# Kernel optimization log

Hardware: AMD Instinct MI355X
Metric: run time of the kernel (lower is better)

## Reference

```python
import jax, jax.numpy as jnp
import numpy as np
import math

DIM = 2048
NUM_HEADS = 32
HEAD_DIM = DIM // NUM_HEADS  # 64; HEAD_DIM//2 == NUM_HEADS (required by original rope broadcasting)
SEQ_LEN = 2048
BATCH = 2
ROPE_BASE = 10000.0


def apply_rope(inputs, positions):
    # Faithful to original: positions is [L]; sinusoid broadcasts to [1, L, H/2, 1]
    # and then multiplies [B, L, N, H/2] -- the original code relies on N == H/2.
    head_dim = inputs.shape[-1]
    fraction = 2.0 * jnp.arange(head_dim // 2, dtype=inputs.dtype) / head_dim
    timescale = ROPE_BASE ** fraction                      # [H/2]
    sinusoid = positions[:, None] / timescale[None, None, :]  # [1, L, H/2]
    sinusoid = sinusoid[..., None]                         # [1, L, H/2, 1]
    sin = jnp.sin(sinusoid)
    cos = jnp.cos(sinusoid)
    first, second = jnp.split(inputs, 2, axis=-1)          # each [B, L, N, H/2]
    return jnp.concatenate([first * cos - second * sin,
                            second * cos + first * sin], axis=-1)


def setup_inputs() -> dict:
    key = jax.random.key(0)
    ks = jax.random.split(key, 9)
    s = 0.02
    inp = {
        'x': jax.random.normal(ks[0], (BATCH, SEQ_LEN, DIM), dtype=jnp.float32),
        'wq_w': jax.random.normal(ks[1], (DIM, DIM), dtype=jnp.float32) * s,
        'wq_b': jnp.zeros((DIM,), dtype=jnp.float32),
        'wk_w': jax.random.normal(ks[2], (DIM, DIM), dtype=jnp.float32) * s,
        'wk_b': jnp.zeros((DIM,), dtype=jnp.float32),
        'wv_w': jax.random.normal(ks[3], (DIM, DIM), dtype=jnp.float32) * s,
        'wv_b': jnp.zeros((DIM,), dtype=jnp.float32),
        'wo_w': jax.random.normal(ks[4], (DIM, DIM), dtype=jnp.float32) * s,
        'wo_b': jnp.zeros((DIM,), dtype=jnp.float32),
    }
    return inp


def reference(x, wq_w, wq_b, wk_w, wk_b, wv_w, wv_b, wo_w, wo_b):
    B, L, _ = x.shape
    N, H = NUM_HEADS, HEAD_DIM
    q = (x @ wq_w.T + wq_b).reshape(B, L, N, H)
    k = (x @ wk_w.T + wk_b).reshape(B, L, N, H)
    v = (x @ wv_w.T + wv_b).reshape(B, L, N, H)
    positions = jnp.arange(L, dtype=x.dtype)
    q = apply_rope(q, positions)
    k = apply_rope(k, positions)
    # [B, N, L, H]
    q = q.transpose(0, 2, 1, 3)
    k = k.transpose(0, 2, 1, 3)
    v = v.transpose(0, 2, 1, 3)
    scale = math.sqrt(H)
    scores = jnp.einsum('bnqh,bnkh->bnqk', q, k) / scale   # [B, N, L, L]
    causal = jnp.tril(jnp.ones((L, L), dtype=bool))
    scores = jnp.where(causal[None, None], scores, -jnp.inf)
    attn = jax.nn.softmax(scores, axis=-1)
    context = jnp.einsum('bnqk,bnkh->bnqh', attn, v)        # [B, N, L, H]
    context = context.transpose(0, 2, 1, 3).reshape(B, L, DIM)
    return context @ wo_w.T + wo_b
```

## Files before the change

### kernel.cpp

```cpp
#include <hip/hip_runtime.h>
#include <stdint.h>

#define D_MODEL 2048
#define SEQLEN  2048

typedef float f32x4  __attribute__((ext_vector_type(4)));
typedef float f32x16 __attribute__((ext_vector_type(16)));
typedef int   i32x4  __attribute__((ext_vector_type(4)));
typedef short s16x4  __attribute__((ext_vector_type(4)));
typedef __bf16 bf16x8 __attribute__((ext_vector_type(8)));

__device__ __forceinline__ unsigned short f2bf(float f) {
  union { float f; uint32_t u; } x; x.f = f;
  uint32_t r = (x.u + 0x7FFFu + ((x.u >> 16) & 1u)) >> 16;
  return (unsigned short)r;
}

__device__ __forceinline__ uint32_t cvtpk(float lo, float hi) {
  uint32_t r;
  asm("v_cvt_pk_bf16_f32 %0, %1, %2" : "=v"(r) : "v"(lo), "v"(hi));
  return r;
}

__device__ __forceinline__ bf16x8 as_bf16x8(i32x4 v) {
  union { i32x4 i; bf16x8 b; } u; u.i = v; return u.b;
}

#define MFMA16(acc, a, b) \
  acc = __builtin_amdgcn_mfma_f32_16x16x32_bf16(as_bf16x8(a), as_bf16x8(b), acc, 0, 0, 0)
#define MFMA32(acc, a, b) \
  acc = __builtin_amdgcn_mfma_f32_32x32x16_bf16(as_bf16x8(a), as_bf16x8(b), acc, 0, 0, 0)

__device__ __forceinline__ void gload16(const void* g, void* lds) {
  __builtin_amdgcn_global_load_lds(
      (const __attribute__((address_space(1))) unsigned int*)(uintptr_t)g,
      (__attribute__((address_space(3))) unsigned int*)(uint32_t)(uintptr_t)lds,
      16, 0, 0);
}

__global__ void cvt_bf16_k(const float* __restrict__ in,
                           unsigned short* __restrict__ out, int n4) {
  int i = blockIdx.x * 256 + threadIdx.x;
  if (i < n4) {
    f32x4 v = *(const f32x4*)&in[(size_t)i * 4];
    s16x4 o;
#pragma unroll
    for (int j = 0; j < 4; ++j) o[j] = (short)f2bf(v[j]);
    *(s16x4*)&out[(size_t)i * 4] = o;
  }
}

template <int MODE>
__global__ __launch_bounds__(512) void gemm4p(
    const unsigned short* __restrict__ A,
    const unsigned short* __restrict__ W0,
    const unsigned short* __restrict__ W1,
    const unsigned short* __restrict__ W2,
    const float* __restrict__ bias0,
    const float* __restrict__ bias1,
    const float* __restrict__ bias2,
    unsigned short* __restrict__ O0,
    unsigned short* __restrict__ O1,
    unsigned short* __restrict__ O2,
    float* __restrict__ Of) {
  constexpr int PLANE_E = 384 * 32;
  __shared__ alignas(16) unsigned short L[4 * PLANE_E];

  const int t = threadIdx.x;
  const int w = t >> 6, l = t & 63;
  const int wm = w >> 1, wn = w & 1;
  const int band = l >> 4, ln = l & 15;

  const int bx = blockIdx.x;
  const int m0 = blockIdx.y * 256;

  const unsigned short* Wm;
  const float* bias;
  int nloc, mat;
  if constexpr (MODE == 0) {
    mat = bx >> 4;
    nloc = (bx & 15) * 128;
    Wm = mat == 0 ? W0 : (mat == 1 ? W1 : W2);
    bias = mat == 0 ? bias0 : (mat == 1 ? bias1 : bias2);
  } else {
    mat = 0;
    nloc = bx * 128;
    Wm = W0;
    bias = bias0;
  }

  auto stage1 = [&](int p, int ktile, int b, int i) {
    unsigned short* dst = L + (b * 2 + p) * PLANE_E;
    const int idx = w * 3 + i;
    const int row = idx * 16 + (l >> 2);
    const int gblk = (l & 3) ^ ((row >> 1) & 3);
    const int kcol = ktile * 64 + p * 32;
    const unsigned short* src =
        (idx < 16) ? &A[(size_t)(m0 + row) * D_MODEL + kcol + gblk * 8]
                   : &Wm[(size_t)(nloc + row - 256) * D_MODEL + kcol + gblk * 8];
    gload16(src, dst + idx * 512);
  };
  auto ld = [&](const unsigned short* pl, int r) {
    return *(const i32x4*)&pl[r * 32 + (((band ^ (r >> 1)) & 3) << 3)];
  };

  f32x4 acc[4][4] = {};

#pragma unroll
  for (int i = 0; i < 3; ++i) stage1(0, 0, 0, i);
#pragma unroll
  for (int i = 0; i < 3; ++i) stage1(1, 0, 0, i);
  asm volatile("s_waitcnt vmcnt(3)" ::: "memory");
  __builtin_amdgcn_s_barrier();

  for (int kt = 0; kt < 32; ++kt) {
    const int rb = kt & 1;
    const int ktn = (kt + 1) & 31;
#pragma unroll
    for (int kh = 0; kh < 2; ++kh) {
      const unsigned short* pl = L + (rb * 2 + kh) * PLANE_E;
      i32x4 bv[4], av[2];
#pragma unroll
      for (int nf = 0; nf < 4; ++nf) bv[nf] = ld(pl, 256 + wn * 64 + nf * 16 + ln);
#pragma unroll
      for (int mf = 0; mf < 2; ++mf) av[mf] = ld(pl, wm * 64 + mf * 16 + ln);
      stage1(kh, ktn, rb ^ 1, 0);
      stage1(kh, ktn, rb ^ 1, 1);
      __builtin_amdgcn_s_barrier();
      asm volatile("s_waitcnt lgkmcnt(0)" ::: "memory");
      __builtin_amdgcn_sched_barrier(0);
      __builtin_amdgcn_s_setprio(1);
#pragma unroll
      for (int mf = 0; mf < 2; ++mf)
#pragma unroll
        for (int nf = 0; nf < 4; ++nf)
          MFMA16(acc[mf][nf], av[mf], bv[nf]);
      __builtin_amdgcn_s_setprio(0);
      __builtin_amdgcn_s_barrier();
#pragma unroll
      for (int mf = 0; mf < 2; ++mf) av[mf] = ld(pl, wm * 64 + (2 + mf) * 16 + ln);
      stage1(kh, ktn, rb ^ 1, 2);
      __builtin_amdgcn_s_barrier();
      asm volatile("s_waitcnt lgkmcnt(0)" ::: "memory");
      __builtin_amdgcn_sched_barrier(0);
      __builtin_amdgcn_s_setprio(1);
#pragma unroll
      for (int mf = 0; mf < 2; ++mf)
#pragma unroll
        for (int nf = 0; nf < 4; ++nf)
          MFMA16(acc[2 + mf][nf], av[mf], bv[nf]);
      __builtin_amdgcn_s_setprio(0);
      asm volatile("s_waitcnt vmcnt(3)" ::: "memory");
      __builtin_amdgcn_s_barrier();
    }
  }
  asm volatile("s_waitcnt vmcnt(0)" ::: "memory");

  float bb[4];
#pragma unroll
  for (int nf = 0; nf < 4; ++nf) bb[nf] = bias[nloc + wn * 64 + nf * 16 + ln];

  if constexpr (MODE == 0) {
    unsigned short* Out = mat == 0 ? O0 : (mat == 1 ? O1 : O2);
    const bool rope = (mat < 2);
    const int head = (nloc + wn * 64) >> 6;
    const float ts = powf(10000.0f, (float)head * (1.0f / 32.0f));
#pragma unroll
    for (int am = 0; am < 4; ++am) {
#pragma unroll
      for (int r = 0; r < 4; ++r) {
        const int row = m0 + wm * 64 + am * 16 + band * 4 + r;
        float vals[4];
#pragma unroll
        for (int nf = 0; nf < 4; ++nf) vals[nf] = acc[am][nf][r] + bb[nf];
        if (rope) {
          const float pos = (float)(row & (SEQLEN - 1));
          float sv, cv;
          sincosf(pos / ts, &sv, &cv);
#pragma unroll
          for (int pp = 0; pp < 2; ++pp) {
            const float f0 = vals[pp], s0 = vals[pp + 2];
            vals[pp]     = f0 * cv - s0 * sv;
            vals[pp + 2] = s0 * cv + f0 * sv;
          }
        }
#pragma unroll
        for (int nf = 0; nf < 4; ++nf)
          Out[(size_t)row * D_MODEL + nloc + wn * 64 + nf * 16 + ln] = f2bf(vals[nf]);
      }
    }
  } else {
#pragma unroll
    for (int am = 0; am < 4; ++am)
#pragma unroll
      for (int r = 0; r < 4; ++r) {
        const int row = m0 + wm * 64 + am * 16 + band * 4 + r;
#pragma unroll
        for (int nf = 0; nf < 4; ++nf)
          Of[(size_t)row * D_MODEL + nloc + wn * 64 + nf * 16 + ln] =
              acc[am][nf][r] + bb[nf];
      }
  }
}

__global__ __launch_bounds__(256) void attn_fwd(
    const unsigned short* __restrict__ Q, const unsigned short* __restrict__ K,
    const unsigned short* __restrict__ V, unsigned short* __restrict__ O) {
  __shared__ alignas(16) unsigned short Ks[2][64 * 64];
  __shared__ alignas(16) unsigned short Vt[2][64 * 80];

  const int t = threadIdx.x;
  const int w = t >> 6, l = t & 63;
  const int l31 = l & 31, t5 = l >> 5;
  const int bx = blockIdx.x, head = blockIdx.y, b = blockIdx.z;
  const int h0 = head * 64;
  const size_t rb = (size_t)b * SEQLEN;

  const int vg = t & 7, vrow = t >> 3;
  const int kdr = l >> 3, kdb = l & 7;

  for (int pi = 0; pi < 2; ++pi) {
    const int qt = pi ? (15 - bx) : bx;
    const int q0 = qt * 128;
    const int qg = q0 + w * 32 + l31;

    i32x4 qf[4];
#pragma unroll
    for (int hk = 0; hk < 4; ++hk)
      qf[hk] = *(const i32x4*)&Q[(rb + qg) * D_MODEL + h0 + hk * 16 + t5 * 8];

    f32x16 oacc[2] = {};
    float lsum = 0.f;
    const int nkt = qt * 2 + 2;

    {
#pragma unroll
      for (int i = 0; i < 2; ++i) {
        const int drow = (i * 4 + w) * 8 + kdr;
        const int sblk = kdb ^ (drow & 7);
        gload16(&K[(rb + drow) * D_MODEL + h0 + sblk * 8], &Ks[0][(i * 4 + w) * 512]);
      }
      i32x4 vv[2];
#pragma unroll
      for (int i = 0; i < 2; ++i)
        vv[i] = *(const i32x4*)&V[(rb + i * 32 + vrow) * D_MODEL + h0 + vg * 8];
      asm volatile("s_waitcnt vmcnt(0)" ::: "memory");
#pragma unroll
      for (int i = 0; i < 2; ++i) {
        const int r = i * 32 + vrow, c8 = vg * 8;
        union { i32x4 v; unsigned short s[8]; } u; u.v = vv[i];
#pragma unroll
        for (int j = 0; j < 8; ++j) Vt[0][(c8 + j) * 80 + (r ^ c8)] = u.s[j];
      }
    }
    __syncthreads();

    for (int kt = 0; kt < nkt; ++kt) {
      const int cur = kt & 1, nxt = cur ^ 1;
      const int k0 = kt * 64;
      const bool more = (kt + 1 < nkt);

      i32x4 vv[2];
      if (more) {
        const int k1 = k0 + 64;
#pragma unroll
        for (int i = 0; i < 2; ++i) {
          const int drow = (i * 4 + w) * 8 + kdr;
          const int sblk = kdb ^ (drow & 7);
          gload16(&K[(rb + k1 + drow) * D_MODEL + h0 + sblk * 8],
                  &Ks[nxt][(i * 4 + w) * 512]);
        }
#pragma unroll
        for (int i = 0; i < 2; ++i)
          vv[i] = *(const i32x4*)&V[(rb + k1 + i * 32 + vrow) * D_MODEL + h0 + vg * 8];
      }

      f32x16 sacc[2] = {};
#pragma unroll
      for (int kvf = 0; kvf < 2; ++kvf) {
        const int krow = kvf * 32 + l31;
#pragma unroll
        for (int hk = 0; hk < 4; ++hk) {
          i32x4 a = *(const i32x4*)&Ks[cur][krow * 64 + ((2 * hk + t5) ^ (krow & 7)) * 8];
          MFMA32(sacc[kvf], a, qf[hk]);
        }
      }

      const bool needmask = (k0 + 64 > q0 + w * 32);
      uint32_t W[2][4][2];
#pragma unroll
      for (int kvf = 0; kvf < 2; ++kvf)
#pragma unroll
        for (int g = 0; g < 4; ++g)
#pragma unroll
          for (int p = 0; p < 2; ++p) {
            float pv[2];
#pragma unroll
            for (int e = 0; e < 2; ++e) {
              const int reg = 4 * g + 2 * p + e;
              const int kvl = kvf * 32 + 8 * g + 4 * t5 + 2 * p + e;
              pv[e] = __expf(sacc[kvf][reg] * 0.125f);
              if (needmask && (k0 + kvl > qg)) pv[e] = 0.f;
              lsum += pv[e];
            }
            W[kvf][g][p] = cvtpk(pv[0], pv[1]);
          }

#pragma unroll
      for (int ks = 0; ks < 4; ++ks) {
        const int kvf = ks >> 1;
        const int gA = 2 * (ks & 1), gB = gA + 1;
        uint32_t a0 = W[kvf][gA][0], b0 = W[kvf][gB][0];
        uint32_t a1 = W[kvf][gA][1], b1 = W[kvf][gB][1];
        asm("v_permlane32_swap_b32 %0, %1" : "+v"(a0), "+v"(b0));
        asm("v_permlane32_swap_b32 %0, %1" : "+v"(a1), "+v"(b1));
        i32x4 pf;
        pf[0] = (int)a0; pf[1] = (int)a1; pf[2] = (int)b0; pf[3] = (int)b1;
#pragma unroll
        for (int hf = 0; hf < 2; ++hf) {
          const int h = hf * 32 + l31;
          i32x4 vb = *(const i32x4*)&Vt[cur][h * 80 + ((ks * 16 + t5 * 8) ^ ((h >> 3) * 8))];
          MFMA32(oacc[hf], pf, vb);
        }
      }

      if (more) {
        asm volatile("s_waitcnt vmcnt(0)" ::: "memory");
#pragma unroll
        for (int i = 0; i < 2; ++i) {
          const int r = i * 32 + vrow, c8 = vg * 8;
          union { i32x4 v; unsigned short s[8]; } u; u.v = vv[i];
#pragma unroll
          for (int j = 0; j < 8; ++j) Vt[nxt][(c8 + j) * 80 + (r ^ c8)] = u.s[j];
        }
      }
      __syncthreads();
    }

    lsum += __shfl_xor(lsum, 32);
    const float inv = 1.0f / lsum;

#pragma unroll
    for (int g2 = 0; g2 < 4; ++g2)
#pragma unroll
      for (int rr = 0; rr < 4; ++rr) {
        const int rowl = rr + 8 * g2 + 4 * t5;
        const float invr = __shfl(inv, (l & 32) + rowl);
        const size_t gr = rb + q0 + w * 32 + rowl;
#pragma unroll
        for (int hf = 0; hf < 2; ++hf)
          O[gr * D_MODEL + h0 + hf * 32 + l31] = f2bf(oacc[hf][4 * g2 + rr] * invr);
      }
  }
}

extern "C" void kernel_launch(void* const* d_in, const int* in_sizes, int n_in,
                              void* d_out, int out_size, void* d_ws, size_t ws_size,
                              hipStream_t stream) {
  const float* x    = (const float*)d_in[0];
  const float* wq_w = (const float*)d_in[1];
  const float* wq_b = (const float*)d_in[2];
  const float* wk_w = (const float*)d_in[3];
  const float* wk_b = (const float*)d_in[4];
  const float* wv_w = (const float*)d_in[5];
  const float* wv_b = (const float*)d_in[6];
  const float* wo_w = (const float*)d_in[7];
  const float* wo_b = (const float*)d_in[8];
  float* out = (float*)d_out;

  unsigned short* ws  = (unsigned short*)d_ws;
  unsigned short* xb  = ws;
  unsigned short* wqb = xb  + 8388608;
  unsigned short* wkb = wqb + 4194304;
  unsigned short* wvb = wkb + 4194304;
  unsigned short* wob = wvb + 4194304;
  unsigned short* qb  = wob + 4194304;
  unsigned short* kb  = qb  + 8388608;
  unsigned short* vb  = kb  + 8388608;
  unsigned short* cb  = xb;

  cvt_bf16_k<<<8192, 256, 0, stream>>>(x, xb, 2097152);
  cvt_bf16_k<<<4096, 256, 0, stream>>>(wq_w, wqb, 1048576);
  cvt_bf16_k<<<4096, 256, 0, stream>>>(wk_w, wkb, 1048576);
  cvt_bf16_k<<<4096, 256, 0, stream>>>(wv_w, wvb, 1048576);
  cvt_bf16_k<<<4096, 256, 0, stream>>>(wo_w, wob, 1048576);

  gemm4p<0><<<dim3(48, 16), 512, 0, stream>>>(
      xb, wqb, wkb, wvb, wq_b, wk_b, wv_b, qb, kb, vb, nullptr);

  attn_fwd<<<dim3(8, 32, 2), 256, 0, stream>>>(qb, kb, vb, cb);

  gemm4p<1><<<dim3(16, 16), 512, 0, stream>>>(
      cb, wob, nullptr, nullptr, wo_b, nullptr, nullptr,
      nullptr, nullptr, nullptr, out);
}
```

Measured before the change: 268.0 us.

## Restructure GEMM to 256 threads with triple-buffered full-K-tile LDS pipeline

New measurement: 331.7 us. 1.24x slower.

```diff
diff --git a/kernel.cpp b/kernel.cpp
--- a/kernel.cpp
+++ b/kernel.cpp
@@ -51,7 +51,7 @@
 }
 
 template <int MODE>
-__global__ __launch_bounds__(512) void gemm4p(
+__global__ __launch_bounds__(256) void gemm3b(
     const unsigned short* __restrict__ A,
     const unsigned short* __restrict__ W0,
     const unsigned short* __restrict__ W1,
@@ -63,8 +63,8 @@
     unsigned short* __restrict__ O1,
     unsigned short* __restrict__ O2,
     float* __restrict__ Of) {
-  constexpr int PLANE_E = 384 * 32;
-  __shared__ alignas(16) unsigned short L[4 * PLANE_E];
+  constexpr int BUF_E = 384 * 64;
+  __shared__ alignas(16) unsigned short L[3 * BUF_E];
 
   const int t = threadIdx.x;
   const int w = t >> 6, l = t & 63;
@@ -89,70 +89,69 @@
     bias = bias0;
   }
 
-  auto stage1 = [&](int p, int ktile, int b, int i) {
-    unsigned short* dst = L + (b * 2 + p) * PLANE_E;
-    const int idx = w * 3 + i;
-    const int row = idx * 16 + (l >> 2);
-    const int gblk = (l & 3) ^ ((row >> 1) & 3);
-    const int kcol = ktile * 64 + p * 32;
-    const unsigned short* src =
-        (idx < 16) ? &A[(size_t)(m0 + row) * D_MODEL + kcol + gblk * 8]
-                   : &Wm[(size_t)(nloc + row - 256) * D_MODEL + kcol + gblk * 8];
-    gload16(src, dst + idx * 512);
+  const int gs = (t & 7) ^ ((t >> 3) & 7);
+  auto stage3 = [&](int b, int ktile, int ph) {
+    const int kcol = ktile * 64 + gs * 8;
+#pragma unroll
+    for (int i = 0; i < 3; ++i) {
+      const int j = ph * 3 + i;
+      const int lin = j * 256 + t;
+      const int row = lin >> 3;
+      const unsigned short* src =
+          (row < 256) ? &A[(size_t)(m0 + row) * D_MODEL + kcol]
+                      : &Wm[(size_t)(nloc + row - 256) * D_MODEL + kcol];
+      gload16(src, &L[b * BUF_E + lin * 8]);
+    }
   };
-  auto ld = [&](const unsigned short* pl, int r) {
-    return *(const i32x4*)&pl[r * 32 + (((band ^ (r >> 1)) & 3) << 3)];
+  auto lda = [&](int b, int row, int slot) {
+    return *(const i32x4*)&L[b * BUF_E + row * 64 + ((slot ^ (row & 7)) << 3)];
   };
 
-  f32x4 acc[4][4] = {};
-
-#pragma unroll
-  for (int i = 0; i < 3; ++i) stage1(0, 0, 0, i);
-#pragma unroll
-  for (int i = 0; i < 3; ++i) stage1(1, 0, 0, i);
-  asm volatile("s_waitcnt vmcnt(3)" ::: "memory");
+  f32x4 acc[8][4] = {};
+
+#pragma unroll
+  for (int ph = 0; ph < 4; ++ph) stage3(0, 0, ph);
+#pragma unroll
+  for (int ph = 0; ph < 4; ++ph) stage3(1, 1, ph);
+  asm volatile("s_waitcnt vmcnt(12)" ::: "memory");
   __builtin_amdgcn_s_barrier();
 
+  int bt = 0;
   for (int kt = 0; kt < 32; ++kt) {
-    const int rb = kt & 1;
-    const int ktn = (kt + 1) & 31;
-#pragma unroll
-    for (int kh = 0; kh < 2; ++kh) {
-      const unsigned short* pl = L + (rb * 2 + kh) * PLANE_E;
-      i32x4 bv[4], av[2];
-#pragma unroll
-      for (int nf = 0; nf < 4; ++nf) bv[nf] = ld(pl, 256 + wn * 64 + nf * 16 + ln);
-#pragma unroll
-      for (int mf = 0; mf < 2; ++mf) av[mf] = ld(pl, wm * 64 + mf * 16 + ln);
-      stage1(kh, ktn, rb ^ 1, 0);
-      stage1(kh, ktn, rb ^ 1, 1);
+    const int bs = (bt >= 1) ? (bt - 1) : (bt + 2);
+    const int stn = (kt + 2) & 31;
+    i32x4 bv[4];
+#pragma unroll
+    for (int ph = 0; ph < 4; ++ph) {
+      const int ks = ph >> 1, hf = ph & 1;
+      i32x4 av[4];
+      if (hf == 0) {
+#pragma unroll
+        for (int nf = 0; nf < 4; ++nf)
+          bv[nf] = lda(bt, 256 + wn * 64 + nf * 16 + ln, ks * 4 + band);
+#pragma unroll
+        for (int mf = 0; mf < 4; ++mf)
+          av[mf] = lda(bt, wm * 128 + mf * 16 + ln, ks * 4 + band);
+      } else {
+#pragma unroll
+        for (int mf = 0; mf < 4; ++mf)
+          av[mf] = lda(bt, wm * 128 + (4 + mf) * 16 + ln, ks * 4 + band);
+      }
+      stage3(bs, stn, ph);
       __builtin_amdgcn_s_barrier();
       asm volatile("s_waitcnt lgkmcnt(0)" ::: "memory");
       __builtin_amdgcn_sched_barrier(0);
       __builtin_amdgcn_s_setprio(1);
 #pragma unroll
-      for (int mf = 0; mf < 2; ++mf)
+      for (int mf = 0; mf < 4; ++mf)
 #pragma unroll
         for (int nf = 0; nf < 4; ++nf)
-          MFMA16(acc[mf][nf], av[mf], bv[nf]);
+          MFMA16(acc[hf * 4 + mf][nf], av[mf], bv[nf]);
       __builtin_amdgcn_s_setprio(0);
+      if (ph == 3) asm volatile("s_waitcnt vmcnt(12)" ::: "memory");
       __builtin_amdgcn_s_barrier();
-#pragma unroll
-      for (int mf = 0; mf < 2; ++mf) av[mf] = ld(pl, wm * 64 + (2 + mf) * 16 + ln);
-      stage1(kh, ktn, rb ^ 1, 2);
-      __builtin_amdgcn_s_barrier();
-      asm volatile("s_waitcnt lgkmcnt(0)" ::: "memory");
-      __builtin_amdgcn_sched_barrier(0);
-      __builtin_amdgcn_s_setprio(1);
-#pragma unroll
-      for (int mf = 0; mf < 2; ++mf)
-#pragma unroll
-        for (int nf = 0; nf < 4; ++nf)
-          MFMA16(acc[2 + mf][nf], av[mf], bv[nf]);
-      __builtin_amdgcn_s_setprio(0);
-      asm volatile("s_waitcnt vmcnt(3)" ::: "memory");
-      __builtin_amdgcn_s_barrier();
-    }
+    }
+    bt = (bt == 2) ? 0 : bt + 1;
   }
   asm volatile("s_waitcnt vmcnt(0)" ::: "memory");
 
@@ -166,10 +165,10 @@
     const int head = (nloc + wn * 64) >> 6;
     const float ts = powf(10000.0f, (float)head * (1.0f / 32.0f));
 #pragma unroll
-    for (int am = 0; am < 4; ++am) {
+    for (int am = 0; am < 8; ++am) {
 #pragma unroll
       for (int r = 0; r < 4; ++r) {
-        const int row = m0 + wm * 64 + am * 16 + band * 4 + r;
+        const int row = m0 + wm * 128 + am * 16 + band * 4 + r;
         float vals[4];
 #pragma unroll
         for (int nf = 0; nf < 4; ++nf) vals[nf] = acc[am][nf][r] + bb[nf];
@@ -191,10 +190,10 @@
     }
   } else {
 #pragma unroll
-    for (int am = 0; am < 4; ++am)
+    for (int am = 0; am < 8; ++am)
 #pragma unroll
       for (int r = 0; r < 4; ++r) {
-        const int row = m0 + wm * 64 + am * 16 + band * 4 + r;
+        const int row = m0 + wm * 128 + am * 16 + band * 4 + r;
 #pragma unroll
         for (int nf = 0; nf < 4; ++nf)
           Of[(size_t)row * D_MODEL + nloc + wn * 64 + nf * 16 + ln] =
@@ -385,12 +384,12 @@
   cvt_bf16_k<<<4096, 256, 0, stream>>>(wv_w, wvb, 1048576);
   cvt_bf16_k<<<4096, 256, 0, stream>>>(wo_w, wob, 1048576);
 
-  gemm4p<0><<<dim3(48, 16), 512, 0, stream>>>(
+  gemm3b<0><<<dim3(48, 16), 256, 0, stream>>>(
       xb, wqb, wkb, wvb, wq_b, wk_b, wv_b, qb, kb, vb, nullptr);
 
   attn_fwd<<<dim3(8, 32, 2), 256, 0, stream>>>(qb, kb, vb, cb);
 
-  gemm4p<1><<<dim3(16, 16), 512, 0, stream>>>(
+  gemm3b<1><<<dim3(16, 16), 256, 0, stream>>>(
       cb, wob, nullptr, nullptr, wo_b, nullptr, nullptr,
       nullptr, nullptr, nullptr, out);
 }
```

## Use 256x256 tiles for QKV GEMM and fuse fp32-to-bf16 conversions

Applied to the files above, without the earlier changes.

Result: slower. 276.2 us (+3.1%).

```diff
diff --git a/kernel.cpp b/kernel.cpp
--- a/kernel.cpp
+++ b/kernel.cpp
@@ -38,20 +38,29 @@
       16, 0, 0);
 }
 
-__global__ void cvt_bf16_k(const float* __restrict__ in,
-                           unsigned short* __restrict__ out, int n4) {
-  int i = blockIdx.x * 256 + threadIdx.x;
-  if (i < n4) {
-    f32x4 v = *(const f32x4*)&in[(size_t)i * 4];
-    s16x4 o;
-#pragma unroll
-    for (int j = 0; j < 4; ++j) o[j] = (short)f2bf(v[j]);
-    *(s16x4*)&out[(size_t)i * 4] = o;
+__global__ void cvt_all_k(const float* __restrict__ x,
+                          const float* __restrict__ w0, const float* __restrict__ w1,
+                          const float* __restrict__ w2, const float* __restrict__ w3,
+                          unsigned short* __restrict__ xo,
+                          unsigned short* __restrict__ o0, unsigned short* __restrict__ o1,
+                          unsigned short* __restrict__ o2, unsigned short* __restrict__ o3) {
+  const int i = blockIdx.x * 256 + threadIdx.x;
+  const float* src; unsigned short* dst; int off;
+  if (i < 2097152) { src = x; dst = xo; off = i; }
+  else {
+    const int j = i - 2097152, seg = j >> 20;
+    off = j & 1048575;
+    src = seg == 0 ? w0 : seg == 1 ? w1 : seg == 2 ? w2 : w3;
+    dst = seg == 0 ? o0 : seg == 1 ? o1 : seg == 2 ? o2 : o3;
   }
-}
-
-template <int MODE>
-__global__ __launch_bounds__(512) void gemm4p(
+  f32x4 v = *(const f32x4*)&src[(size_t)off * 4];
+  s16x4 o;
+#pragma unroll
+  for (int j = 0; j < 4; ++j) o[j] = (short)f2bf(v[j]);
+  *(s16x4*)&dst[(size_t)off * 4] = o;
+}
+
+__global__ __launch_bounds__(512) void gemm256(
     const unsigned short* __restrict__ A,
     const unsigned short* __restrict__ W0,
     const unsigned short* __restrict__ W1,
@@ -61,7 +70,147 @@
     const float* __restrict__ bias2,
     unsigned short* __restrict__ O0,
     unsigned short* __restrict__ O1,
-    unsigned short* __restrict__ O2,
+    unsigned short* __restrict__ O2) {
+  __shared__ alignas(16) unsigned short L[2][512 * 64];
+
+  const int t = threadIdx.x;
+  const int w = t >> 6, l = t & 63;
+  const int wm = w >> 2, wn = w & 3;
+  const int band = l >> 4, ln = l & 15;
+
+  const int bx = blockIdx.x;
+  const int m0 = blockIdx.y * 256;
+  const int mat = bx >> 3;
+  const int nloc = (bx & 7) * 256;
+  const unsigned short* Wm = mat == 0 ? W0 : (mat == 1 ? W1 : W2);
+  const float* bias = mat == 0 ? bias0 : (mat == 1 ? bias1 : bias2);
+
+  auto stage = [&](int b, int ktile, int h) {
+#pragma unroll
+    for (int j = 0; j < 2; ++j) {
+      const int lin = (w * 2 + j) * 64 + l;
+      const int rowh = lin >> 3, s = lin & 7;
+      const int row = h * 128 + rowh;
+      const int kcol = ktile * 64 + ((s ^ (rowh & 7)) << 3);
+      const unsigned short* src =
+          (row < 256) ? &A[(size_t)(m0 + row) * D_MODEL + kcol]
+                      : &Wm[(size_t)(nloc + row - 256) * D_MODEL + kcol];
+      gload16(src, &L[b][h * 8192 + lin * 8]);
+    }
+  };
+  auto lda = [&](int b, int row, int slot) {
+    return *(const i32x4*)&L[b][row * 64 + ((slot ^ (row & 7)) << 3)];
+  };
+
+  f32x4 acc[8][4] = {};
+
+#pragma unroll
+  for (int h = 0; h < 4; ++h) stage(0, 0, h);
+#pragma unroll
+  for (int h = 0; h < 4; ++h) stage(1, 1, h);
+  asm volatile("s_waitcnt vmcnt(8)" ::: "memory");
+  __builtin_amdgcn_s_barrier();
+
+  for (int kt = 0; kt < 32; ++kt) {
+    const int rb = kt & 1;
+    const int stn = (kt + 2) & 31;
+    i32x4 av[4], bv[4];
+#pragma unroll
+    for (int nf = 0; nf < 4; ++nf) bv[nf] = lda(rb, 256 + wn * 64 + nf * 16 + ln, band);
+#pragma unroll
+    for (int mf = 0; mf < 4; ++mf) av[mf] = lda(rb, wm * 128 + mf * 16 + ln, band);
+    __builtin_amdgcn_s_barrier();
+    asm volatile("s_waitcnt lgkmcnt(0)" ::: "memory");
+    __builtin_amdgcn_sched_barrier(0);
+    __builtin_amdgcn_s_setprio(1);
+#pragma unroll
+    for (int mf = 0; mf < 4; ++mf)
+#pragma unroll
+      for (int nf = 0; nf < 4; ++nf) MFMA16(acc[mf][nf], av[mf], bv[nf]);
+    __builtin_amdgcn_s_setprio(0);
+    __builtin_amdgcn_s_barrier();
+#pragma unroll
+    for (int mf = 0; mf < 4; ++mf) av[mf] = lda(rb, wm * 128 + (4 + mf) * 16 + ln, band);
+    __builtin_amdgcn_s_barrier();
+    asm volatile("s_waitcnt lgkmcnt(0)" ::: "memory");
+    __builtin_amdgcn_sched_barrier(0);
+    __builtin_amdgcn_s_setprio(1);
+#pragma unroll
+    for (int mf = 0; mf < 4; ++mf)
+#pragma unroll
+      for (int nf = 0; nf < 4; ++nf) MFMA16(acc[4 + mf][nf], av[mf], bv[nf]);
+    __builtin_amdgcn_s_setprio(0);
+    __builtin_amdgcn_s_barrier();
+#pragma unroll
+    for (int nf = 0; nf < 4; ++nf) bv[nf] = lda(rb, 256 + wn * 64 + nf * 16 + ln, 4 + band);
+#pragma unroll
+    for (int mf = 0; mf < 4; ++mf) av[mf] = lda(rb, wm * 128 + mf * 16 + ln, 4 + band);
+    __builtin_amdgcn_s_barrier();
+    asm volatile("s_waitcnt lgkmcnt(0)" ::: "memory");
+    __builtin_amdgcn_sched_barrier(0);
+    __builtin_amdgcn_s_setprio(1);
+#pragma unroll
+    for (int mf = 0; mf < 4; ++mf)
+#pragma unroll
+      for (int nf = 0; nf < 4; ++nf) MFMA16(acc[mf][nf], av[mf], bv[nf]);
+    __builtin_amdgcn_s_setprio(0);
+    __builtin_amdgcn_s_barrier();
+#pragma unroll
+    for (int mf = 0; mf < 4; ++mf) av[mf] = lda(rb, wm * 128 + (4 + mf) * 16 + ln, 4 + band);
+    __builtin_amdgcn_s_barrier();
+    asm volatile("s_waitcnt lgkmcnt(0)" ::: "memory");
+    __builtin_amdgcn_sched_barrier(0);
+#pragma unroll
+    for (int h = 0; h < 4; ++h) stage(rb, stn, h);
+    __builtin_amdgcn_s_setprio(1);
+#pragma unroll
+    for (int mf = 0; mf < 4; ++mf)
+#pragma unroll
+      for (int nf = 0; nf < 4; ++nf) MFMA16(acc[4 + mf][nf], av[mf], bv[nf]);
+    __builtin_amdgcn_s_setprio(0);
+    asm volatile("s_waitcnt vmcnt(8)" ::: "memory");
+    __builtin_amdgcn_s_barrier();
+  }
+  asm volatile("s_waitcnt vmcnt(0)" ::: "memory");
+
+  float bb[4];
+#pragma unroll
+  for (int nf = 0; nf < 4; ++nf) bb[nf] = bias[nloc + wn * 64 + nf * 16 + ln];
+
+  unsigned short* Out = mat == 0 ? O0 : (mat == 1 ? O1 : O2);
+  const bool rope = (mat < 2);
+  const int head = (nloc >> 6) + wn;
+  const float ts = powf(10000.0f, (float)head * (1.0f / 32.0f));
+#pragma unroll
+  for (int am = 0; am < 8; ++am) {
+#pragma unroll
+    for (int r = 0; r < 4; ++r) {
+      const int row = m0 + wm * 128 + am * 16 + band * 4 + r;
+      float vals[4];
+#pragma unroll
+      for (int nf = 0; nf < 4; ++nf) vals[nf] = acc[am][nf][r] + bb[nf];
+      if (rope) {
+        const float pos = (float)(row & (SEQLEN - 1));
+        float sv, cv;
+        sincosf(pos / ts, &sv, &cv);
+#pragma unroll
+        for (int pp = 0; pp < 2; ++pp) {
+          const float f0 = vals[pp], s0 = vals[pp + 2];
+          vals[pp]     = f0 * cv - s0 * sv;
+          vals[pp + 2] = s0 * cv + f0 * sv;
+        }
+      }
+#pragma unroll
+      for (int nf = 0; nf < 4; ++nf)
+        Out[(size_t)row * D_MODEL + nloc + wn * 64 + nf * 16 + ln] = f2bf(vals[nf]);
+    }
+  }
+}
+
+__global__ __launch_bounds__(512) void gemmop(
+    const unsigned short* __restrict__ A,
+    const unsigned short* __restrict__ W0,
+    const float* __restrict__ bias0,
     float* __restrict__ Of) {
   constexpr int PLANE_E = 384 * 32;
   __shared__ alignas(16) unsigned short L[4 * PLANE_E];
@@ -71,23 +220,8 @@
   const int wm = w >> 1, wn = w & 1;
   const int band = l >> 4, ln = l & 15;
 
-  const int bx = blockIdx.x;
   const int m0 = blockIdx.y * 256;
-
-  const unsigned short* Wm;
-  const float* bias;
-  int nloc, mat;
-  if constexpr (MODE == 0) {
-    mat = bx >> 4;
-    nloc = (bx & 15) * 128;
-    Wm = mat == 0 ? W0 : (mat == 1 ? W1 : W2);
-    bias = mat == 0 ? bias0 : (mat == 1 ? bias1 : bias2);
-  } else {
-    mat = 0;
-    nloc = bx * 128;
-    Wm = W0;
-    bias = bias0;
-  }
+  const int nloc = blockIdx.x * 128;
 
   auto stage1 = [&](int p, int ktile, int b, int i) {
     unsigned short* dst = L + (b * 2 + p) * PLANE_E;
@@ -97,7 +231,7 @@
     const int kcol = ktile * 64 + p * 32;
     const unsigned short* src =
         (idx < 16) ? &A[(size_t)(m0 + row) * D_MODEL + kcol + gblk * 8]
-                   : &Wm[(size_t)(nloc + row - 256) * D_MODEL + kcol + gblk * 8];
+                   : &W0[(size_t)(nloc + row - 256) * D_MODEL + kcol + gblk * 8];
     gload16(src, dst + idx * 512);
   };
   auto ld = [&](const unsigned short* pl, int r) {
@@ -133,8 +267,7 @@
 #pragma unroll
       for (int mf = 0; mf < 2; ++mf)
 #pragma unroll
-        for (int nf = 0; nf < 4; ++nf)
-          MFMA16(acc[mf][nf], av[mf], bv[nf]);
+        for (int nf = 0; nf < 4; ++nf) MFMA16(acc[mf][nf], av[mf], bv[nf]);
       __builtin_amdgcn_s_setprio(0);
       __builtin_amdgcn_s_barrier();
 #pragma unroll
@@ -147,8 +280,7 @@
 #pragma unroll
       for (int mf = 0; mf < 2; ++mf)
 #pragma unroll
-        for (int nf = 0; nf < 4; ++nf)
-          MFMA16(acc[2 + mf][nf], av[mf], bv[nf]);
+        for (int nf = 0; nf < 4; ++nf) MFMA16(acc[2 + mf][nf], av[mf], bv[nf]);
       __builtin_amdgcn_s_setprio(0);
       asm volatile("s_waitcnt vmcnt(3)" ::: "memory");
       __builtin_amdgcn_s_barrier();
@@ -158,49 +290,17 @@
 
   float bb[4];
 #pragma unroll
-  for (int nf = 0; nf < 4; ++nf) bb[nf] = bias[nloc + wn * 64 + nf * 16 + ln];
-
-  if constexpr (MODE == 0) {
-    unsigned short* Out = mat == 0 ? O0 : (mat == 1 ? O1 : O2);
-    const bool rope = (mat < 2);
-    const int head = (nloc + wn * 64) >> 6;
-    const float ts = powf(10000.0f, (float)head * (1.0f / 32.0f));
-#pragma unroll
-    for (int am = 0; am < 4; ++am) {
-#pragma unroll
-      for (int r = 0; r < 4; ++r) {
-        const int row = m0 + wm * 64 + am * 16 + band * 4 + r;
-        float vals[4];
-#pragma unroll
-        for (int nf = 0; nf < 4; ++nf) vals[nf] = acc[am][nf][r] + bb[nf];
-        if (rope) {
-          const float pos = (float)(row & (SEQLEN - 1));
-          float sv, cv;
-          sincosf(pos / ts, &sv, &cv);
-#pragma unroll
-          for (int pp = 0; pp < 2; ++pp) {
-            const float f0 = vals[pp], s0 = vals[pp + 2];
-            vals[pp]     = f0 * cv - s0 * sv;
-            vals[pp + 2] = s0 * cv + f0 * sv;
-          }
-        }
-#pragma unroll
-        for (int nf = 0; nf < 4; ++nf)
-          Out[(size_t)row * D_MODEL + nloc + wn * 64 + nf * 16 + ln] = f2bf(vals[nf]);
-      }
-    }
-  } else {
-#pragma unroll
-    for (int am = 0; am < 4; ++am)
-#pragma unroll
-      for (int r = 0; r < 4; ++r) {
-        const int row = m0 + wm * 64 + am * 16 + band * 4 + r;
-#pragma unroll
-        for (int nf = 0; nf < 4; ++nf)
-          Of[(size_t)row * D_MODEL + nloc + wn * 64 + nf * 16 + ln] =
-              acc[am][nf][r] + bb[nf];
-      }
-  }
+  for (int nf = 0; nf < 4; ++nf) bb[nf] = bias0[nloc + wn * 64 + nf * 16 + ln];
+#pragma unroll
+  for (int am = 0; am < 4; ++am)
+#pragma unroll
+    for (int r = 0; r < 4; ++r) {
+      const int row = m0 + wm * 64 + am * 16 + band * 4 + r;
+#pragma unroll
+      for (int nf = 0; nf < 4; ++nf)
+        Of[(size_t)row * D_MODEL + nloc + wn * 64 + nf * 16 + ln] =
+            acc[am][nf][r] + bb[nf];
+    }
 }
 
 __global__ __launch_bounds__(256) void attn_fwd(
@@ -379,18 +479,13 @@
   unsigned short* vb  = kb  + 8388608;
   unsigned short* cb  = xb;
 
-  cvt_bf16_k<<<8192, 256, 0, stream>>>(x, xb, 2097152);
-  cvt_bf16_k<<<4096, 256, 0, stream>>>(wq_w, wqb, 1048576);
-  cvt_bf16_k<<<4096, 256, 0, stream>>>(wk_w, wkb, 1048576);
-  cvt_bf16_k<<<4096, 256, 0, stream>>>(wv_w, wvb, 1048576);
-  cvt_bf16_k<<<4096, 256, 0, stream>>>(wo_w, wob, 1048576);
-
-  gemm4p<0><<<dim3(48, 16), 512, 0, stream>>>(
-      xb, wqb, wkb, wvb, wq_b, wk_b, wv_b, qb, kb, vb, nullptr);
+  cvt_all_k<<<24576, 256, 0, stream>>>(x, wq_w, wk_w, wv_w, wo_w,
+                                       xb, wqb, wkb, wvb, wob);
+
+  gemm256<<<dim3(24, 16), 512, 0, stream>>>(
+      xb, wqb, wkb, wvb, wq_b, wk_b, wv_b, qb, kb, vb);
 
   attn_fwd<<<dim3(8, 32, 2), 256, 0, stream>>>(qb, kb, vb, cb);
 
-  gemm4p<1><<<dim3(16, 16), 512, 0, stream>>>(
-      cb, wob, nullptr, nullptr, wo_b, nullptr, nullptr,
-      nullptr, nullptr, nullptr, out);
-}
+  gemmop<<<dim3(16, 16), 512, 0, stream>>>(cb, wob, wo_b, out);
+}
```

## Merge bf16 conversions into one launch and split fused QKV GEMM per matrix

Applied to the files above, without the earlier changes.

Result: no change. 264.7 us (-1.2%).

```diff
diff --git a/kernel.cpp b/kernel.cpp
--- a/kernel.cpp
+++ b/kernel.cpp
@@ -38,30 +38,34 @@
       16, 0, 0);
 }
 
-__global__ void cvt_bf16_k(const float* __restrict__ in,
-                           unsigned short* __restrict__ out, int n4) {
-  int i = blockIdx.x * 256 + threadIdx.x;
-  if (i < n4) {
-    f32x4 v = *(const f32x4*)&in[(size_t)i * 4];
-    s16x4 o;
-#pragma unroll
-    for (int j = 0; j < 4; ++j) o[j] = (short)f2bf(v[j]);
-    *(s16x4*)&out[(size_t)i * 4] = o;
+__global__ void cvt_all_k(const float* __restrict__ x,
+                          const float* __restrict__ w0, const float* __restrict__ w1,
+                          const float* __restrict__ w2, const float* __restrict__ w3,
+                          unsigned short* __restrict__ xo,
+                          unsigned short* __restrict__ o0, unsigned short* __restrict__ o1,
+                          unsigned short* __restrict__ o2, unsigned short* __restrict__ o3) {
+  const int i = blockIdx.x * 256 + threadIdx.x;
+  const float* src; unsigned short* dst; int off;
+  if (i < 2097152) { src = x; dst = xo; off = i; }
+  else {
+    const int j = i - 2097152, seg = j >> 20;
+    off = j & 1048575;
+    src = seg == 0 ? w0 : seg == 1 ? w1 : seg == 2 ? w2 : w3;
+    dst = seg == 0 ? o0 : seg == 1 ? o1 : seg == 2 ? o2 : o3;
   }
-}
-
-template <int MODE>
-__global__ __launch_bounds__(512) void gemm4p(
+  f32x4 v = *(const f32x4*)&src[(size_t)off * 4];
+  s16x4 o;
+#pragma unroll
+  for (int j = 0; j < 4; ++j) o[j] = (short)f2bf(v[j]);
+  *(s16x4*)&dst[(size_t)off * 4] = o;
+}
+
+template <bool ROPE, bool F32OUT>
+__global__ __launch_bounds__(512) void gemm1(
     const unsigned short* __restrict__ A,
-    const unsigned short* __restrict__ W0,
-    const unsigned short* __restrict__ W1,
-    const unsigned short* __restrict__ W2,
-    const float* __restrict__ bias0,
-    const float* __restrict__ bias1,
-    const float* __restrict__ bias2,
-    unsigned short* __restrict__ O0,
-    unsigned short* __restrict__ O1,
-    unsigned short* __restrict__ O2,
+    const unsigned short* __restrict__ W,
+    const float* __restrict__ bias,
+    unsigned short* __restrict__ Ob,
     float* __restrict__ Of) {
   constexpr int PLANE_E = 384 * 32;
   __shared__ alignas(16) unsigned short L[4 * PLANE_E];
@@ -71,23 +75,8 @@
   const int wm = w >> 1, wn = w & 1;
   const int band = l >> 4, ln = l & 15;
 
-  const int bx = blockIdx.x;
   const int m0 = blockIdx.y * 256;
-
-  const unsigned short* Wm;
-  const float* bias;
-  int nloc, mat;
-  if constexpr (MODE == 0) {
-    mat = bx >> 4;
-    nloc = (bx & 15) * 128;
-    Wm = mat == 0 ? W0 : (mat == 1 ? W1 : W2);
-    bias = mat == 0 ? bias0 : (mat == 1 ? bias1 : bias2);
-  } else {
-    mat = 0;
-    nloc = bx * 128;
-    Wm = W0;
-    bias = bias0;
-  }
+  const int nloc = blockIdx.x * 128;
 
   auto stage1 = [&](int p, int ktile, int b, int i) {
     unsigned short* dst = L + (b * 2 + p) * PLANE_E;
@@ -97,7 +86,7 @@
     const int kcol = ktile * 64 + p * 32;
     const unsigned short* src =
         (idx < 16) ? &A[(size_t)(m0 + row) * D_MODEL + kcol + gblk * 8]
-                   : &Wm[(size_t)(nloc + row - 256) * D_MODEL + kcol + gblk * 8];
+                   : &W[(size_t)(nloc + row - 256) * D_MODEL + kcol + gblk * 8];
     gload16(src, dst + idx * 512);
   };
   auto ld = [&](const unsigned short* pl, int r) {
@@ -133,8 +122,7 @@
 #pragma unroll
       for (int mf = 0; mf < 2; ++mf)
 #pragma unroll
-        for (int nf = 0; nf < 4; ++nf)
-          MFMA16(acc[mf][nf], av[mf], bv[nf]);
+        for (int nf = 0; nf < 4; ++nf) MFMA16(acc[mf][nf], av[mf], bv[nf]);
       __builtin_amdgcn_s_setprio(0);
       __builtin_amdgcn_s_barrier();
 #pragma unroll
@@ -147,8 +135,7 @@
 #pragma unroll
       for (int mf = 0; mf < 2; ++mf)
 #pragma unroll
-        for (int nf = 0; nf < 4; ++nf)
-          MFMA16(acc[2 + mf][nf], av[mf], bv[nf]);
+        for (int nf = 0; nf < 4; ++nf) MFMA16(acc[2 + mf][nf], av[mf], bv[nf]);
       __builtin_amdgcn_s_setprio(0);
       asm volatile("s_waitcnt vmcnt(3)" ::: "memory");
       __builtin_amdgcn_s_barrier();
@@ -160,46 +147,34 @@
 #pragma unroll
   for (int nf = 0; nf < 4; ++nf) bb[nf] = bias[nloc + wn * 64 + nf * 16 + ln];
 
-  if constexpr (MODE == 0) {
-    unsigned short* Out = mat == 0 ? O0 : (mat == 1 ? O1 : O2);
-    const bool rope = (mat < 2);
-    const int head = (nloc + wn * 64) >> 6;
-    const float ts = powf(10000.0f, (float)head * (1.0f / 32.0f));
-#pragma unroll
-    for (int am = 0; am < 4; ++am) {
-#pragma unroll
-      for (int r = 0; r < 4; ++r) {
-        const int row = m0 + wm * 64 + am * 16 + band * 4 + r;
-        float vals[4];
-#pragma unroll
-        for (int nf = 0; nf < 4; ++nf) vals[nf] = acc[am][nf][r] + bb[nf];
-        if (rope) {
-          const float pos = (float)(row & (SEQLEN - 1));
-          float sv, cv;
-          sincosf(pos / ts, &sv, &cv);
-#pragma unroll
-          for (int pp = 0; pp < 2; ++pp) {
-            const float f0 = vals[pp], s0 = vals[pp + 2];
-            vals[pp]     = f0 * cv - s0 * sv;
-            vals[pp + 2] = s0 * cv + f0 * sv;
-          }
-        }
-#pragma unroll
-        for (int nf = 0; nf < 4; ++nf)
-          Out[(size_t)row * D_MODEL + nloc + wn * 64 + nf * 16 + ln] = f2bf(vals[nf]);
+  const int head = (nloc + wn * 64) >> 6;
+  const float ts = powf(10000.0f, (float)head * (1.0f / 32.0f));
+#pragma unroll
+  for (int am = 0; am < 4; ++am) {
+#pragma unroll
+    for (int r = 0; r < 4; ++r) {
+      const int row = m0 + wm * 64 + am * 16 + band * 4 + r;
+      float vals[4];
+#pragma unroll
+      for (int nf = 0; nf < 4; ++nf) vals[nf] = acc[am][nf][r] + bb[nf];
+      if constexpr (ROPE) {
+        const float pos = (float)(row & (SEQLEN - 1));
+        float sv, cv;
+        __sincosf(pos / ts, &sv, &cv);
+#pragma unroll
+        for (int pp = 0; pp < 2; ++pp) {
+          const float f0 = vals[pp], s0 = vals[pp + 2];
+          vals[pp]     = f0 * cv - s0 * sv;
+          vals[pp + 2] = s0 * cv + f0 * sv;
+        }
+      }
+#pragma unroll
+      for (int nf = 0; nf < 4; ++nf) {
+        const size_t oi = (size_t)row * D_MODEL + nloc + wn * 64 + nf * 16 + ln;
+        if constexpr (F32OUT) Of[oi] = vals[nf];
+        else                  Ob[oi] = f2bf(vals[nf]);
       }
     }
-  } else {
-#pragma unroll
-    for (int am = 0; am < 4; ++am)
-#pragma unroll
-      for (int r = 0; r < 4; ++r) {
-        const int row = m0 + wm * 64 + am * 16 + band * 4 + r;
-#pragma unroll
-        for (int nf = 0; nf < 4; ++nf)
-          Of[(size_t)row * D_MODEL + nloc + wn * 64 + nf * 16 + ln] =
-              acc[am][nf][r] + bb[nf];
-      }
   }
 }
 
@@ -379,18 +354,15 @@
   unsigned short* vb  = kb  + 8388608;
   unsigned short* cb  = xb;
 
-  cvt_bf16_k<<<8192, 256, 0, stream>>>(x, xb, 2097152);
-  cvt_bf16_k<<<4096, 256, 0, stream>>>(wq_w, wqb, 1048576);
-  cvt_bf16_k<<<4096, 256, 0, stream>>>(wk_w, wkb, 1048576);
-  cvt_bf16_k<<<4096, 256, 0, stream>>>(wv_w, wvb, 1048576);
-  cvt_bf16_k<<<4096, 256, 0, stream>>>(wo_w, wob, 1048576);
-
-  gemm4p<0><<<dim3(48, 16), 512, 0, stream>>>(
-      xb, wqb, wkb, wvb, wq_b, wk_b, wv_b, qb, kb, vb, nullptr);
+  cvt_all_k<<<24576, 256, 0, stream>>>(x, wq_w, wk_w, wv_w, wo_w,
+                                       xb, wqb, wkb, wvb, wob);
+
+  dim3 g(16, 16);
+  gemm1<true,  false><<<g, 512, 0, stream>>>(xb, wqb, wq_b, qb, nullptr);
+  gemm1<true,  false><<<g, 512, 0, stream>>>(xb, wkb, wk_b, kb, nullptr);
+  gemm1<false, false><<<g, 512, 0, stream>>>(xb, wvb, wv_b, vb, nullptr);
 
   attn_fwd<<<dim3(8, 32, 2), 256, 0, stream>>>(qb, kb, vb, cb);
 
-  gemm4p<1><<<dim3(16, 16), 512, 0, stream>>>(
-      cb, wob, nullptr, nullptr, wo_b, nullptr, nullptr,
-      nullptr, nullptr, nullptr, out);
-}
+  gemm1<false, true><<<g, 512, 0, stream>>>(cb, wob, wo_b, nullptr, out);
+}
```
